# Performance work log

Measured on AMD Instinct MI355X. Metric: run time of the kernel, lower is better.

## Reference

```python
import jax, jax.numpy as jnp
import numpy as np
from jax import lax

B, DIM, H, W = 2, 64, 64, 64
HEADS = 4  # hardcoded in FuseNet (SpectralBlock(dim,4), RestormerBlock(dim,4))
EPS_LN = 1e-5


def pw(x, w, b=None):
    # 1x1 conv, NCHW; w: (out, in)
    y = jnp.einsum('bihw,oi->bohw', x, w)
    return y if b is None else y + b[None, :, None, None]


def dw(x, w, b=None):
    # depthwise 3x3 conv; w: (C, 1, 3, 3)
    y = lax.conv_general_dilated(x, w, (1, 1), 'SAME',
                                 feature_group_count=x.shape[1],
                                 dimension_numbers=('NCHW', 'OIHW', 'NCHW'))
    return y if b is None else y + b[None, :, None, None]


def ln_biasfree(x, w):
    # BiasFree_LayerNorm over channel dim of NCHW (matches to_3d -> var over c)
    mu = jnp.mean(x, axis=1, keepdims=True)
    var = jnp.mean((x - mu) ** 2, axis=1, keepdims=True)
    return x / jnp.sqrt(var + EPS_LN) * w[None, :, None, None]


def ffn(x, in_w, dw_w, out_w):
    # FeedForward: 1x1 -> dw3x3 -> chunk -> gelu gate -> 1x1 (all bias=False)
    h2 = dw(pw(x, in_w), dw_w)
    x1, x2 = jnp.split(h2, 2, axis=1)
    return pw(jax.nn.gelu(x1, approximate=False) * x2, out_w)


def restormer_attn(x, qkv_w, qkv_dw_w, proj_w, temp):
    b, c, h, w = x.shape
    qkv = dw(pw(x, qkv_w), qkv_dw_w)
    q, k, v = jnp.split(qkv, 3, axis=1)
    rs = lambda t: t.reshape(b, HEADS, c // HEADS, h * w)
    q, k, v = rs(q), rs(k), rs(v)
    q = q / jnp.maximum(jnp.linalg.norm(q, axis=-1, keepdims=True), 1e-12)
    k = k / jnp.maximum(jnp.linalg.norm(k, axis=-1, keepdims=True), 1e-12)
    attn = jax.nn.softmax(jnp.einsum('bhcn,bhdn->bhcd', q, k) * temp[None], axis=-1)
    out = jnp.einsum('bhcd,bhdn->bhcn', attn, v).reshape(b, c, h, w)
    return pw(out, proj_w)


def cross_attn(q4, k4, v4, qw, qb, kw, kb, vw, vb, ow, ob):
    b, c, h, w = q4.shape
    n, hd = h * w, c // HEADS
    tok = lambda t: t.reshape(b, c, n).transpose(0, 2, 1)  # b n c
    Q = (jnp.einsum('bnc,oc->bno', tok(q4), qw) + qb).reshape(b, n, HEADS, hd)
    K = (jnp.einsum('bnc,oc->bno', tok(k4), kw) + kb).reshape(b, n, HEADS, hd)
    V = (jnp.einsum('bnc,oc->bno', tok(v4), vw) + vb).reshape(b, n, HEADS, hd)
    energy = jnp.einsum('bqhd,bkhd->bhqk', Q, K)
    attn = jax.nn.softmax(energy / jnp.sqrt(jnp.float32(hd)), axis=-1)
    out = jnp.einsum('bhqk,bkhd->bqhd', attn, V).reshape(b, n, c)
    out = jnp.einsum('bnc,oc->bno', out, ow) + ob
    return out.transpose(0, 2, 1).reshape(b, c, h, w)


def setup_inputs() -> dict:
    key = jax.random.key(0)
    ks = jax.random.split(key, 48)
    d = DIM
    nrm = lambda i, shape, s=0.05: (jax.random.normal(ks[i], shape, jnp.float32) * s)
    inp = {
        'hsi_f0': nrm(0, (B, d, H, W), 1.0),
        'msi_f0': nrm(1, (B, d, H, W), 1.0),
        'hsi_fi': nrm(2, (B, d, H, W), 1.0),
        'msi_fi': nrm(3, (B, d, H, W), 1.0),
        # FuseNet score MLPs (1x1 convs, bias=True)
        'sp_mlp_w': nrm(4, (d, 1)), 'sp_mlp_b': nrm(5, (d,)),
        'spe_mlp_w': nrm(6, (d, d)), 'spe_mlp_b': nrm(7, (d,)),
        # spatial/spectral conv branches (bias=True defaults)
        'spa_dw_w': nrm(8, (d, 1, 3, 3)), 'spa_dw_b': nrm(9, (d,)),
        'spa_pw_w': nrm(10, (d, d)), 'spa_pw_b': nrm(11, (d,)),
        'spe_dw_w': nrm(12, (d, 1, 3, 3)), 'spe_dw_b': nrm(13, (d,)),
        'spe_pw_w': nrm(14, (d, d)), 'spe_pw_b': nrm(15, (d,)),
        # SpectralBlock: CrossAttention linears (bias=True) + norm2 + FFN (bias=False)
        'sb_q_w': nrm(16, (d, d)), 'sb_q_b': nrm(17, (d,)),
        'sb_k_w': nrm(18, (d, d)), 'sb_k_b': nrm(19, (d,)),
        'sb_v_w': nrm(20, (d, d)), 'sb_v_b': nrm(21, (d,)),
        'sb_o_w': nrm(22, (d, d)), 'sb_o_b': nrm(23, (d,)),
        'sb_norm2_w': jnp.ones((d,), jnp.float32),
        'sb_ffn_in_w': nrm(24, (2 * d, d)),
        'sb_ffn_dw_w': nrm(25, (2 * d, 1, 3, 3)),
        'sb_ffn_out_w': nrm(26, (d, d)),
        # RestormerBlock
        'rb_norm1_w': jnp.ones((d,), jnp.float32),
        'rb_temp': jnp.ones((HEADS, 1, 1), jnp.float32),
        'rb_qkv_w': nrm(27, (3 * d, d)),
        'rb_qkv_dw_w': nrm(28, (3 * d, 1, 3, 3)),
        'rb_proj_w': nrm(29, (d, d)),
        'rb_norm2_w': jnp.ones((d,), jnp.float32),
        'rb_ffn_in_w': nrm(30, (2 * d, d)),
        'rb_ffn_dw_w': nrm(31, (2 * d, 1, 3, 3)),
        'rb_ffn_out_w': nrm(32, (d, d)),
    }
    return inp


def reference(hsi_f0, msi_f0, hsi_fi, msi_fi,
              sp_mlp_w, sp_mlp_b, spe_mlp_w, spe_mlp_b,
              spa_dw_w, spa_dw_b, spa_pw_w, spa_pw_b,
              spe_dw_w, spe_dw_b, spe_pw_w, spe_pw_b,
              sb_q_w, sb_q_b, sb_k_w, sb_k_b, sb_v_w, sb_v_b, sb_o_w, sb_o_b,
              sb_norm2_w, sb_ffn_in_w, sb_ffn_dw_w, sb_ffn_out_w,
              rb_norm1_w, rb_temp, rb_qkv_w, rb_qkv_dw_w, rb_proj_w,
              rb_norm2_w, rb_ffn_in_w, rb_ffn_dw_w, rb_ffn_out_w):
    relu6 = lambda t: jnp.clip(t, 0.0, 6.0)
    # spectral score: global max-pool over HW, 1x1 conv, relu6
    spectral_score = jnp.max(hsi_fi, axis=(2, 3), keepdims=True)
    spectral_score = relu6(pw(spectral_score, spe_mlp_w, spe_mlp_b))
    # spatial score: channel mean, 1x1 conv (1->dim), relu6
    spatial_score = jnp.mean(msi_fi, axis=1, keepdims=True)
    spatial_score = relu6(pw(spatial_score, sp_mlp_w, sp_mlp_b))
    # spectral branch on hsi_f0
    hsi = dw(hsi_f0, spe_dw_w, spe_dw_b)
    hsi = hsi + jnp.clip(spectral_score, -1.0, 1.0)
    hsi = pw(hsi, spe_pw_w, spe_pw_b)
    # spatial branch on msi_f0
    msi = dw(msi_f0, spa_dw_w, spa_dw_b)
    msi = msi + jnp.clip(spatial_score, -1.0, 1.0)
    msi = pw(msi, spa_pw_w, spa_pw_b)
    # SpectralBlock: x = cross_attn(q,k,v) + q; x = x + ffn(ln(x))
    x1 = cross_attn(msi, hsi, hsi, sb_q_w, sb_q_b, sb_k_w, sb_k_b,
                    sb_v_w, sb_v_b, sb_o_w, sb_o_b) + msi
    x1 = x1 + ffn(ln_biasfree(x1, sb_norm2_w), sb_ffn_in_w, sb_ffn_dw_w, sb_ffn_out_w)
    # RestormerBlock on msi + hsi
    y = msi + hsi
    y = y + restormer_attn(ln_biasfree(y, rb_norm1_w), rb_qkv_w, rb_qkv_dw_w, rb_proj_w, rb_temp)
    x2 = y + ffn(ln_biasfree(y, rb_norm2_w), rb_ffn_in_w, rb_ffn_dw_w, rb_ffn_out_w)
    return x1 + x2
```

## Files before the change

### kernel.cpp

```cpp
#include <hip/hip_runtime.h>
#include <hip/hip_bf16.h>

#define NB 2
#define NC 64
#define NHW 4096
#define NPIX (NB*NHW)
#define SZ   (NB*NC*NHW)

typedef __attribute__((ext_vector_type(8))) short bf16x8;
typedef __attribute__((ext_vector_type(4))) float f32x4;
typedef __hip_bfloat16 hbf;

__device__ __forceinline__ float clamp01(float v){ return fminf(fmaxf(v, 0.f), 1.f); }

__global__ __launch_bounds__(256) void k_max_hw(const float* __restrict__ in, float* __restrict__ mx){
  int bc = blockIdx.x; int t = threadIdx.x;
  const float* p = in + (size_t)bc*NHW;
  float m = -1e30f;
  for (int n = t; n < NHW; n += 256) m = fmaxf(m, p[n]);
  #pragma unroll
  for (int off = 32; off; off >>= 1) m = fmaxf(m, __shfl_xor(m, off));
  __shared__ float sm[4];
  if ((t & 63) == 0) sm[t >> 6] = m;
  __syncthreads();
  if (t == 0) mx[bc] = fmaxf(fmaxf(sm[0], sm[1]), fmaxf(sm[2], sm[3]));
}

__global__ void k_spe_score(const float* __restrict__ mx, const float* __restrict__ w,
                            const float* __restrict__ bias, float* __restrict__ out){
  int t = threadIdx.x; if (t >= 128) return;
  int b = t >> 6, o = t & 63;
  float acc = bias[o];
  const float* m = mx + b*64;
  for (int i = 0; i < 64; ++i) acc += w[o*64 + i] * m[i];
  out[t] = clamp01(acc);
}

__global__ __launch_bounds__(256) void k_chmean(const float* __restrict__ in, float* __restrict__ out){
  int p = blockIdx.x*256 + threadIdx.x;
  int b = p >> 12, n = p & 4095;
  const float* base = in + (size_t)b*NC*NHW + n;
  float s = 0.f;
  #pragma unroll
  for (int c = 0; c < 64; ++c) s += base[c*NHW];
  out[p] = s * (1.0f/64.0f);
}

__global__ __launch_bounds__(256) void k_dw3b(const float* __restrict__ in0, const float* __restrict__ w0,
    const float* __restrict__ b0, const float* __restrict__ add_bc,
    const float* __restrict__ in1, const float* __restrict__ w1, const float* __restrict__ b1,
    const float* __restrict__ chmean, const float* __restrict__ spw, const float* __restrict__ spb,
    float* __restrict__ out0, float* __restrict__ out1){
  int bb = blockIdx.x;
  int br = bb >= (SZ/256);
  int g = (br ? bb - SZ/256 : bb)*256 + threadIdx.x;
  const float* in = br ? in1 : in0;
  const float* w  = br ? w1  : w0;
  const float* bs = br ? b1  : b0;
  float* out      = br ? out1 : out0;
  int pix = g & 4095; int c = (g >> 12) & 63; int b = g >> 18;
  int y = pix >> 6, x = pix & 63;
  const float* base = in + (size_t)(b*64 + c)*NHW;
  float wf[9];
  #pragma unroll
  for (int i = 0; i < 9; ++i) wf[i] = w[c*9 + i];
  float acc = 0.f;
  #pragma unroll
  for (int ky = -1; ky <= 1; ++ky){
    int yy = y + ky; if ((unsigned)yy >= 64u) continue;
    #pragma unroll
    for (int kx = -1; kx <= 1; ++kx){
      int xx = x + kx; if ((unsigned)xx >= 64u) continue;
      acc += base[yy*64 + xx] * wf[(ky+1)*3 + (kx+1)];
    }
  }
  acc += bs[c];
  if (!br) acc += add_bc[b*64 + c];
  else{
    float z = spw[c] * chmean[b*4096 + pix] + spb[c];
    acc += clamp01(z);
  }
  out[g] = acc;
}

__global__ __launch_bounds__(256) void k_pw(const float* __restrict__ in, const float* __restrict__ w,
    const float* __restrict__ bias, const float* __restrict__ lnw,
    const float* __restrict__ in2, float* __restrict__ add_out,
    const float* __restrict__ r1, const float* __restrict__ r2,
    float* __restrict__ outf, int OC,
    hbf* __restrict__ tq, float tscale, hbf* __restrict__ cq,
    const float* __restrict__ Pacc, const float* __restrict__ Pm, const float* __restrict__ Pl){
  __shared__ __align__(16) float Xs[64][32];
  __shared__ __align__(16) float Wt[64][64];
  __shared__ float psum[8][32], psqs[8][32];
  __shared__ float invs[32];
  __shared__ float fs[4][4][32];
  int t = threadIdx.x;
  int ptile = blockIdx.x; int oc0 = blockIdx.y*64;
  int b = ptile >> 7; int n0 = (ptile & 127)*32;
  const float* inb = in ? in + (size_t)b*64*NHW + n0 : nullptr;
  const float* inb2 = in2 ? in2 + (size_t)b*64*NHW + n0 : nullptr;
  float* aob = add_out ? add_out + (size_t)b*64*NHW + n0 : nullptr;
  if (Pacc){
    if (t < 128){
      int h = t >> 5, n = t & 31;
      int bh = b*4 + h, q = n0 + n;
      float mv[4], lv[4]; float mn = -1e30f;
      #pragma unroll
      for (int c = 0; c < 4; ++c){
        mv[c] = Pm[(size_t)(c*8+bh)*4096 + q];
        lv[c] = Pl[(size_t)(c*8+bh)*4096 + q];
        mn = fmaxf(mn, mv[c]);
      }
      float f[4]; float L = 0.f;
      #pragma unroll
      for (int c = 0; c < 4; ++c){ f[c] = __expf(mv[c]-mn); L += lv[c]*f[c]; }
      float inv = 1.0f / L;
      #pragma unroll
      for (int c = 0; c < 4; ++c) fs[c][h][n] = f[c]*inv;
    }
    __syncthreads();
  }
  float ps = 0.f, pss = 0.f;
  #pragma unroll
  for (int k = 0; k < 8; ++k){
    int i = k*8 + (t >> 5); int n = t & 31;
    float v;
    if (Pacc){
      int h = i >> 4, d = i & 15, bh = b*4 + h;
      const float* pb = Pacc + ((size_t)(bh*16 + d))*4096 + n0 + n;
      v = pb[0]*fs[0][h][n] + pb[(size_t)SZ]*fs[1][h][n]
        + pb[(size_t)2*SZ]*fs[2][h][n] + pb[(size_t)3*SZ]*fs[3][h][n];
    } else {
      v = inb[(size_t)i*NHW + n];
      if (inb2) v += inb2[(size_t)i*NHW + n];
    }
    Xs[i][n] = v;
    if (aob && blockIdx.y == 0) aob[(size_t)i*NHW + n] = v;
    ps += v; pss += v*v;
  }
  if (lnw){ psum[t>>5][t&31] = ps; psqs[t>>5][t&31] = pss; }
  #pragma unroll
  for (int k = 0; k < 16; ++k){
    int idx = k*256 + t; int o = idx & 63, i = idx >> 6;
    float wv = w[(oc0 + o)*64 + i];
    if (lnw) wv *= lnw[i];
    Wt[i][o] = wv;
  }
  __syncthreads();
  if (lnw){
    if (t < 32){
      float s1 = 0.f, s2 = 0.f;
      #pragma unroll
      for (int g = 0; g < 8; ++g){ s1 += psum[g][t]; s2 += psqs[g][t]; }
      float mu = s1*(1.0f/64.0f);
      float var = s2*(1.0f/64.0f) - mu*mu;
      invs[t] = rsqrtf(fmaxf(var, 0.f) + 1e-5f);
    }
    __syncthreads();
  }
  int tn = t & 15, to = t >> 4;
  float a0x=0,a0y=0,a1x=0,a1y=0,a2x=0,a2y=0,a3x=0,a3y=0;
  #pragma unroll
  for (int i = 0; i < 64; ++i){
    const float2 xv = *(const float2*)&Xs[i][tn*2];
    const float4 wv = *(const float4*)&Wt[i][to*4];
    a0x += wv.x*xv.x; a0y += wv.x*xv.y;
    a1x += wv.y*xv.x; a1y += wv.y*xv.y;
    a2x += wv.z*xv.x; a2y += wv.z*xv.y;
    a3x += wv.w*xv.x; a3y += wv.w*xv.y;
  }
  float sx = 1.f, sy = 1.f;
  if (lnw){ sx = invs[tn*2+0]; sy = invs[tn*2+1]; }
  float ax[4] = {a0x,a1x,a2x,a3x}, ay[4] = {a0y,a1y,a2y,a3y};
  #pragma unroll
  for (int oo = 0; oo < 4; ++oo){
    int o = oc0 + to*4 + oo;
    float bv = bias ? bias[o] : 0.f;
    size_t obase = ((size_t)b*OC + o)*NHW + n0 + tn*2;
    float v0 = ax[oo]*sx + bv, v1 = ay[oo]*sy + bv;
    if (r1){ v0 += r1[obase+0]; v1 += r1[obase+1]; }
    if (r2){ v0 += r2[obase+0]; v1 += r2[obase+1]; }
    if (tq){
      int h = o >> 4, d = o & 15;
      size_t tb = ((size_t)(b*4 + h)*4096 + n0 + tn*2)*16 + d;
      tq[tb]    = __float2bfloat16(v0*tscale);
      tq[tb+16] = __float2bfloat16(v1*tscale);
    }
    if (cq){
      cq[obase+0] = __float2bfloat16(v0);
      cq[obase+1] = __float2bfloat16(v1);
    }
    if (outf){
      float2 vv; vv.x = v0; vv.y = v1;
      *(float2*)(outf + obase) = vv;
    }
  }
}

__global__ __launch_bounds__(256) void k_mfa(const hbf* __restrict__ Qt, const hbf* __restrict__ Kt,
                                             const hbf* __restrict__ Vb, float* __restrict__ Pacc,
                                             float* __restrict__ Pm, float* __restrict__ Pl){
  int blk = blockIdx.x;
  int qt = blk & 63; int bh = (blk >> 6) & 7; int c = blk >> 9;
  int t = threadIdx.x;
  int w = t >> 6, l = t & 63;
  int lg = l >> 4, lq = l & 15;
  int q0 = qt*64 + w*16;
  int rho = ((lq >> 2) << 3) + (lq & 3);
  bf16x8 qf = {};
  if (lg < 2) qf = *(const bf16x8*)&Qt[((size_t)bh*4096 + q0 + lq)*16 + lg*8];
  f32x4 acc = {0.f, 0.f, 0.f, 0.f};
  float m = -1e30f, lsum = 0.f;
  const hbf* Ktb = Kt + ((size_t)bh*4096 + c*1024)*16;
  const hbf* Vbb = Vb + (size_t)bh*16*4096 + c*1024;
  for (int kb = 0; kb < 1024; kb += 32){
    bf16x8 kf0 = {}, kf1 = {};
    if (lg < 2){
      kf0 = *(const bf16x8*)&Ktb[(size_t)(kb + rho)*16 + lg*8];
      kf1 = *(const bf16x8*)&Ktb[(size_t)(kb + rho + 4)*16 + lg*8];
    }
    f32x4 z = {0.f, 0.f, 0.f, 0.f};
    f32x4 s0 = __builtin_amdgcn_mfma_f32_16x16x32_bf16(kf0, qf, z, 0, 0, 0);
    f32x4 s1 = __builtin_amdgcn_mfma_f32_16x16x32_bf16(kf1, qf, z, 0, 0, 0);
    float p[8];
    p[0]=s0[0]; p[1]=s0[1]; p[2]=s0[2]; p[3]=s0[3];
    p[4]=s1[0]; p[5]=s1[1]; p[6]=s1[2]; p[7]=s1[3];
    float cm = p[0];
    #pragma unroll
    for (int i = 1; i < 8; ++i) cm = fmaxf(cm, p[i]);
    cm = fmaxf(cm, __shfl_xor(cm, 16));
    cm = fmaxf(cm, __shfl_xor(cm, 32));
    if (!__all(cm <= m + 8.f)){
      float mn = fmaxf(m, cm);
      float f = __expf(m - mn);
      lsum *= f;
      acc[0] *= f; acc[1] *= f; acc[2] *= f; acc[3] *= f;
      m = mn;
    }
    float psum_ = 0.f;
    #pragma unroll
    for (int i = 0; i < 8; ++i){ p[i] = __expf(p[i]-m); psum_ += p[i]; }
    psum_ += __shfl_xor(psum_, 16);
    psum_ += __shfl_xor(psum_, 32);
    lsum += psum_;
    bf16x8 pf;
    #pragma unroll
    for (int j = 0; j < 8; ++j){
      hbf hb = __float2bfloat16(p[j]);
      pf[j] = *reinterpret_cast<short*>(&hb);
    }
    bf16x8 vf = *(const bf16x8*)&Vbb[(size_t)lq*4096 + kb + lg*8];
    acc = __builtin_amdgcn_mfma_f32_16x16x32_bf16(vf, pf, acc, 0, 0, 0);
  }
  int pb = c*8 + bh;
  if (lg == 0){
    Pm[(size_t)pb*4096 + q0 + lq] = m;
    Pl[(size_t)pb*4096 + q0 + lq] = lsum;
  }
  #pragma unroll
  for (int r = 0; r < 4; ++r){
    int d = lg*4 + r;
    Pacc[((size_t)pb*16 + d)*4096 + q0 + lq] = acc[r];
  }
}

__global__ __launch_bounds__(256) void k_dwgate(const float* __restrict__ in, const float* __restrict__ w,
                                                float* __restrict__ out){
  int g = blockIdx.x*256 + threadIdx.x;
  int pix = g & 4095; int c = (g >> 12) & 63; int b = g >> 18;
  int y = pix >> 6, x = pix & 63;
  const float* p1 = in + ((size_t)b*128 + c)*NHW;
  const float* p2 = in + ((size_t)b*128 + 64 + c)*NHW;
  float w1[9], w2[9];
  #pragma unroll
  for (int i = 0; i < 9; ++i){ w1[i] = w[c*9+i]; w2[i] = w[(64+c)*9+i]; }
  float a = 0.f, bb = 0.f;
  #pragma unroll
  for (int ky = -1; ky <= 1; ++ky){
    int yy = y + ky; if ((unsigned)yy >= 64u) continue;
    #pragma unroll
    for (int kx = -1; kx <= 1; ++kx){
      int xx = x + kx; if ((unsigned)xx >= 64u) continue;
      int off = yy*64 + xx; int wi = (ky+1)*3 + (kx+1);
      a  += p1[off]*w1[wi];
      bb += p2[off]*w2[wi];
    }
  }
  float gl = 0.5f*a*(1.0f + erff(a*0.70710678118654752f));
  out[g] = gl*bb;
}

__global__ __launch_bounds__(256) void k_dw192(const float* __restrict__ in, const float* __restrict__ w,
                                               float* __restrict__ out){
  int g = blockIdx.x*256 + threadIdx.x;
  int pix = g & 4095; int bc = g >> 12; int c = bc % 192;
  int y = pix >> 6, x = pix & 63;
  const float* p = in + (size_t)bc*NHW;
  float wf[9];
  #pragma unroll
  for (int i = 0; i < 9; ++i) wf[i] = w[c*9+i];
  float acc = 0.f;
  #pragma unroll
  for (int ky = -1; ky <= 1; ++ky){
    int yy = y + ky; if ((unsigned)yy >= 64u) continue;
    #pragma unroll
    for (int kx = -1; kx <= 1; ++kx){
      int xx = x + kx; if ((unsigned)xx >= 64u) continue;
      acc += p[yy*64 + xx]*wf[(ky+1)*3 + (kx+1)];
    }
  }
  out[g] = acc;
}

__global__ __launch_bounds__(256) void k_rnorm(const float* __restrict__ qkv, float* __restrict__ norms){
  int blk = blockIdx.x; int b = blk >> 7, r = blk & 127;
  int t = threadIdx.x;
  const float* p = qkv + ((size_t)b*192 + r)*NHW;
  float ss = 0.f;
  for (int i = t*4; i < NHW; i += 1024){
    float4 v = *(const float4*)(p + i);
    ss += v.x*v.x + v.y*v.y + v.z*v.z + v.w*v.w;
  }
  #pragma unroll
  for (int off = 32; off; off >>= 1) ss += __shfl_xor(ss, off);
  __shared__ float sm[4];
  if ((t & 63) == 0) sm[t >> 6] = ss;
  __syncthreads();
  if (t == 0) norms[blk] = fmaxf(sqrtf(sm[0]+sm[1]+sm[2]+sm[3]), 1e-12f);
}

__global__ __launch_bounds__(256) void k_rattn2(const float* __restrict__ qkv, const float* __restrict__ norms,
                                                const float* __restrict__ temp, float* __restrict__ out){
  int blk = blockIdx.x; int rq = blk & 15, h = (blk >> 4) & 3, b = blk >> 6;
  int t = threadIdx.x;
  const float* bq = qkv + ((size_t)b*192 + h*16 + rq)*NHW;
  const float* bk = qkv + ((size_t)b*192 + 64 + h*16)*NHW;
  float p[16];
  #pragma unroll
  for (int rk = 0; rk < 16; ++rk) p[rk] = 0.f;
  for (int n = t*4; n < NHW; n += 1024){
    float4 qv4 = *(const float4*)(bq + n);
    #pragma unroll
    for (int rk = 0; rk < 16; ++rk){
      float4 kv = *(const float4*)(bk + (size_t)rk*NHW + n);
      p[rk] += qv4.x*kv.x + qv4.y*kv.y + qv4.z*kv.z + qv4.w*kv.w;
    }
  }
  #pragma unroll
  for (int rk = 0; rk < 16; ++rk)
    #pragma unroll
    for (int off = 32; off; off >>= 1) p[rk] += __shfl_xor(p[rk], off);
  __shared__ float red[4][16];
  if ((t & 63) == 0){
    int wv_ = t >> 6;
    #pragma unroll
    for (int rk = 0; rk < 16; ++rk) red[wv_][rk] = p[rk];
  }
  __syncthreads();
  __shared__ float attn[16];
  if (t == 0){
    float nq = norms[b*128 + h*16 + rq];
    float tp = temp[h];
    float e[16]; float mm = -1e30f;
    #pragma unroll
    for (int rk = 0; rk < 16; ++rk){
      float dot = red[0][rk]+red[1][rk]+red[2][rk]+red[3][rk];
      e[rk] = dot/(nq*norms[b*128 + 64 + h*16 + rk]) * tp;
      mm = fmaxf(mm, e[rk]);
    }
    float ssum = 0.f;
    #pragma unroll
    for (int rk = 0; rk < 16; ++rk){ e[rk] = __expf(e[rk]-mm); ssum += e[rk]; }
    float is = 1.f/ssum;
    #pragma unroll
    for (int rk = 0; rk < 16; ++rk) attn[rk] = e[rk]*is;
  }
  __syncthreads();
  float aw[16];
  #pragma unroll
  for (int rk = 0; rk < 16; ++rk) aw[rk] = attn[rk];
  const float* vb = qkv + ((size_t)b*192 + 128 + h*16)*NHW;
  float* ob = out + ((size_t)b*64 + h*16 + rq)*NHW;
  for (int n = t*4; n < NHW; n += 1024){
    float4 o; o.x = 0.f; o.y = 0.f; o.z = 0.f; o.w = 0.f;
    #pragma unroll
    for (int rk = 0; rk < 16; ++rk){
      float4 v = *(const float4*)(vb + (size_t)rk*NHW + n);
      o.x += aw[rk]*v.x; o.y += aw[rk]*v.y; o.z += aw[rk]*v.z; o.w += aw[rk]*v.w;
    }
    *(float4*)(ob + n) = o;
  }
}

extern "C" void kernel_launch(void* const* d_in, const int* in_sizes, int n_in,
                              void* d_out, int out_size, void* d_ws, size_t ws_size,
                              hipStream_t stream){
  const float* hsi_f0     = (const float*)d_in[0];
  const float* msi_f0     = (const float*)d_in[1];
  const float* hsi_fi     = (const float*)d_in[2];
  const float* msi_fi     = (const float*)d_in[3];
  const float* sp_mlp_w   = (const float*)d_in[4];
  const float* sp_mlp_b   = (const float*)d_in[5];
  const float* spe_mlp_w  = (const float*)d_in[6];
  const float* spe_mlp_b  = (const float*)d_in[7];
  const float* spa_dw_w   = (const float*)d_in[8];
  const float* spa_dw_b   = (const float*)d_in[9];
  const float* spa_pw_w   = (const float*)d_in[10];
  const float* spa_pw_b   = (const float*)d_in[11];
  const float* spe_dw_w   = (const float*)d_in[12];
  const float* spe_dw_b   = (const float*)d_in[13];
  const float* spe_pw_w   = (const float*)d_in[14];
  const float* spe_pw_b   = (const float*)d_in[15];
  const float* sb_q_w     = (const float*)d_in[16];
  const float* sb_q_b     = (const float*)d_in[17];
  const float* sb_k_w     = (const float*)d_in[18];
  const float* sb_k_b     = (const float*)d_in[19];
  const float* sb_v_w     = (const float*)d_in[20];
  const float* sb_v_b     = (const float*)d_in[21];
  const float* sb_o_w     = (const float*)d_in[22];
  const float* sb_o_b     = (const float*)d_in[23];
  const float* sb_norm2_w = (const float*)d_in[24];
  const float* sb_ffn_in_w  = (const float*)d_in[25];
  const float* sb_ffn_dw_w  = (const float*)d_in[26];
  const float* sb_ffn_out_w = (const float*)d_in[27];
  const float* rb_norm1_w = (const float*)d_in[28];
  const float* rb_temp    = (const float*)d_in[29];
  const float* rb_qkv_w   = (const float*)d_in[30];
  const float* rb_qkv_dw_w= (const float*)d_in[31];
  const float* rb_proj_w  = (const float*)d_in[32];
  const float* rb_norm2_w = (const float*)d_in[33];
  const float* rb_ffn_in_w  = (const float*)d_in[34];
  const float* rb_ffn_dw_w  = (const float*)d_in[35];
  const float* rb_ffn_out_w = (const float*)d_in[36];

  float* W   = (float*)d_ws;
  float* Hb  = W;
  float* Mb  = W + (size_t)SZ;
  float* Xb  = W + (size_t)2*SZ;
  float* Yb  = W + (size_t)3*SZ;
  float* T1  = W + (size_t)4*SZ;
  float* QKV = T1;
  float* TB  = W + (size_t)7*SZ;
  float* Tm  = TB;
  float* TB2 = W + (size_t)9*SZ;
  float* Pacc= W + (size_t)7*SZ;
  float* Pm  = W + (size_t)11*SZ;
  float* Pl  = W + (size_t)11*SZ + 131072;
  float* mxb = W + (size_t)12*SZ;
  float* speb= mxb + 128;
  float* cmb = speb + 128;
  float* normb = W + (size_t)12*SZ + 9216;
  hbf* Qt  = (hbf*)(W + (size_t)5*SZ);
  hbf* Kt  = Qt + (size_t)8*4096*16;
  hbf* Vbf = Kt + (size_t)8*4096*16;

  float* outf = (float*)d_out;

  k_max_hw  <<<NB*NC, 256, 0, stream>>>(hsi_fi, mxb);
  k_spe_score<<<1, 128, 0, stream>>>(mxb, spe_mlp_w, spe_mlp_b, speb);
  k_chmean  <<<NPIX/256, 256, 0, stream>>>(msi_fi, cmb);
  k_dw3b<<<2*SZ/256, 256, 0, stream>>>(hsi_f0, spe_dw_w, spe_dw_b, speb,
                                       msi_f0, spa_dw_w, spa_dw_b, cmb, sp_mlp_w, sp_mlp_b,
                                       T1, Tm);
  k_pw<<<dim3(NPIX/32,1), 256, 0, stream>>>(T1, spe_pw_w, spe_pw_b, nullptr, nullptr, nullptr, nullptr, nullptr, Hb, 64, nullptr, 1.f, nullptr, nullptr, nullptr, nullptr);
  k_pw<<<dim3(NPIX/32,1), 256, 0, stream>>>(Tm, spa_pw_w, spa_pw_b, nullptr, nullptr, nullptr, nullptr, nullptr, Mb, 64, nullptr, 1.f, nullptr, nullptr, nullptr, nullptr);
  k_pw<<<dim3(NPIX/32,1), 256, 0, stream>>>(Mb, sb_q_w, sb_q_b, nullptr, nullptr, nullptr, nullptr, nullptr, nullptr, 64, Qt, 0.25f, nullptr, nullptr, nullptr, nullptr);
  k_pw<<<dim3(NPIX/32,1), 256, 0, stream>>>(Hb, sb_k_w, sb_k_b, nullptr, nullptr, nullptr, nullptr, nullptr, nullptr, 64, Kt, 1.f, nullptr, nullptr, nullptr, nullptr);
  k_pw<<<dim3(NPIX/32,1), 256, 0, stream>>>(Hb, sb_v_w, sb_v_b, nullptr, nullptr, nullptr, nullptr, nullptr, nullptr, 64, nullptr, 1.f, Vbf, nullptr, nullptr, nullptr);
  k_mfa<<<2048, 256, 0, stream>>>(Qt, Kt, Vbf, Pacc, Pm, Pl);
  k_pw<<<dim3(NPIX/32,1), 256, 0, stream>>>(nullptr, sb_o_w, sb_o_b, nullptr, nullptr, nullptr, Mb, nullptr, Xb, 64, nullptr, 1.f, nullptr, Pacc, Pm, Pl);
  k_pw<<<dim3(NPIX/32,2), 256, 0, stream>>>(Xb, sb_ffn_in_w, nullptr, sb_norm2_w, nullptr, nullptr, nullptr, nullptr, TB, 128, nullptr, 1.f, nullptr, nullptr, nullptr, nullptr);
  k_dwgate<<<SZ/256, 256, 0, stream>>>(TB, sb_ffn_dw_w, T1);
  k_pw<<<dim3(NPIX/32,1), 256, 0, stream>>>(T1, sb_ffn_out_w, nullptr, nullptr, nullptr, nullptr, Xb, nullptr, Xb, 64, nullptr, 1.f, nullptr, nullptr, nullptr, nullptr);
  k_pw<<<dim3(NPIX/32,3), 256, 0, stream>>>(Hb, rb_qkv_w, nullptr, rb_norm1_w, Mb, Yb, nullptr, nullptr, TB2, 192, nullptr, 1.f, nullptr, nullptr, nullptr, nullptr);
  k_dw192<<<3*SZ/256, 256, 0, stream>>>(TB2, rb_qkv_dw_w, QKV);
  k_rnorm<<<256, 256, 0, stream>>>(QKV, normb);
  k_rattn2<<<128, 256, 0, stream>>>(QKV, normb, rb_temp, TB);
  k_pw<<<dim3(NPIX/32,1), 256, 0, stream>>>(TB, rb_proj_w, nullptr, nullptr, nullptr, nullptr, Yb, nullptr, Yb, 64, nullptr, 1.f, nullptr, nullptr, nullptr, nullptr);
  k_pw<<<dim3(NPIX/32,2), 256, 0, stream>>>(Yb, rb_ffn_in_w, nullptr, rb_norm2_w, nullptr, nullptr, nullptr, nullptr, TB, 128, nullptr, 1.f, nullptr, nullptr, nullptr, nullptr);
  k_dwgate<<<SZ/256, 256, 0, stream>>>(TB, rb_ffn_dw_w, T1);
  k_pw<<<dim3(NPIX/32,1), 256, 0, stream>>>(T1, rb_ffn_out_w, nullptr, nullptr, nullptr, nullptr, Xb, Yb, outf, 64, nullptr, 1.f, nullptr, nullptr, nullptr, nullptr);
}
```

Measured before the change: 276.8 us.

## Batch independent pointwise and depthwise launches, fold spectral MLP, use exp2 softmax

Independent 1x1-conv jobs are grouped into single launches through a job struct indexed by blockIdx.z: the two branch projections, the Q/K/V projections, and the SB FFN-in with the RB QKV projection. The FFN depthwise gate and the 192-channel depthwise conv are merged into one kernel, and the spectral-score MLP is computed inside the depthwise kernel, removing a one-block launch. Softmax now uses exp2f, with log2(e) folded into the Q scale and the rescale threshold. This is meant to cut launch count and fill the GPU better with small grids. The cost is redundant per-thread MLP dot products and buffer reuse (G1 aliases Mb) that must not conflict.

```diff
diff --git a/kernel.cpp b/kernel.cpp
--- a/kernel.cpp
+++ b/kernel.cpp
@@ -6,6 +6,7 @@
 #define NHW 4096
 #define NPIX (NB*NHW)
 #define SZ   (NB*NC*NHW)
+#define LOG2E 1.4426950408889634f
 
 typedef __attribute__((ext_vector_type(8))) short bf16x8;
 typedef __attribute__((ext_vector_type(4))) float f32x4;
@@ -26,16 +27,6 @@
   if (t == 0) mx[bc] = fmaxf(fmaxf(sm[0], sm[1]), fmaxf(sm[2], sm[3]));
 }
 
-__global__ void k_spe_score(const float* __restrict__ mx, const float* __restrict__ w,
-                            const float* __restrict__ bias, float* __restrict__ out){
-  int t = threadIdx.x; if (t >= 128) return;
-  int b = t >> 6, o = t & 63;
-  float acc = bias[o];
-  const float* m = mx + b*64;
-  for (int i = 0; i < 64; ++i) acc += w[o*64 + i] * m[i];
-  out[t] = clamp01(acc);
-}
-
 __global__ __launch_bounds__(256) void k_chmean(const float* __restrict__ in, float* __restrict__ out){
   int p = blockIdx.x*256 + threadIdx.x;
   int b = p >> 12, n = p & 4095;
@@ -46,19 +37,23 @@
   out[p] = s * (1.0f/64.0f);
 }
 
-__global__ __launch_bounds__(256) void k_dw3b(const float* __restrict__ in0, const float* __restrict__ w0,
-    const float* __restrict__ b0, const float* __restrict__ add_bc,
-    const float* __restrict__ in1, const float* __restrict__ w1, const float* __restrict__ b1,
-    const float* __restrict__ chmean, const float* __restrict__ spw, const float* __restrict__ spb,
+__global__ __launch_bounds__(256) void k_dw3b(const float* __restrict__ hsi0, const float* __restrict__ wh,
+    const float* __restrict__ bh, const float* __restrict__ mxb,
+    const float* __restrict__ spe_w, const float* __restrict__ spe_b,
+    const float* __restrict__ msi0, const float* __restrict__ wm, const float* __restrict__ bm,
+    const float* __restrict__ cmb, const float* __restrict__ spw, const float* __restrict__ spb,
     float* __restrict__ out0, float* __restrict__ out1){
   int bb = blockIdx.x;
   int br = bb >= (SZ/256);
-  int g = (br ? bb - SZ/256 : bb)*256 + threadIdx.x;
-  const float* in = br ? in1 : in0;
-  const float* w  = br ? w1  : w0;
-  const float* bs = br ? b1  : b0;
+  int bbl = br ? bb - SZ/256 : bb;
+  int b = bbl >> 10;
+  int c = (bbl >> 4) & 63;
+  int t = threadIdx.x;
+  int pix = (bbl & 15)*256 + t;
+  const float* in = br ? msi0 : hsi0;
+  const float* w  = br ? wm : wh;
+  const float* bs = br ? bm : bh;
   float* out      = br ? out1 : out0;
-  int pix = g & 4095; int c = (g >> 12) & 63; int b = g >> 18;
   int y = pix >> 6, x = pix & 63;
   const float* base = in + (size_t)(b*64 + c)*NHW;
   float wf[9];
@@ -75,32 +70,40 @@
     }
   }
   acc += bs[c];
-  if (!br) acc += add_bc[b*64 + c];
-  else{
-    float z = spw[c] * chmean[b*4096 + pix] + spb[c];
+  if (!br){
+    float spe = spe_b[c];
+    #pragma unroll 8
+    for (int i = 0; i < 64; ++i) spe += spe_w[c*64 + i] * mxb[b*64 + i];
+    acc += clamp01(spe);
+  } else {
+    float z = spw[c] * cmb[b*4096 + pix] + spb[c];
     acc += clamp01(z);
   }
-  out[g] = acc;
-}
-
-__global__ __launch_bounds__(256) void k_pw(const float* __restrict__ in, const float* __restrict__ w,
-    const float* __restrict__ bias, const float* __restrict__ lnw,
-    const float* __restrict__ in2, float* __restrict__ add_out,
-    const float* __restrict__ r1, const float* __restrict__ r2,
-    float* __restrict__ outf, int OC,
-    hbf* __restrict__ tq, float tscale, hbf* __restrict__ cq,
-    const float* __restrict__ Pacc, const float* __restrict__ Pm, const float* __restrict__ Pl){
+  out[(size_t)(b*64 + c)*NHW + pix] = acc;
+}
+
+struct PwJob {
+  const float *in, *w, *bias, *lnw, *in2;
+  float *add_out;
+  const float *r1, *r2;
+  float *outf;
+  int OC;
+  hbf *tq; float tscale; hbf *cq;
+};
+
+__device__ __forceinline__ void pw_body(const PwJob j,
+    const float* __restrict__ Pacc, const float* __restrict__ Pm, const float* __restrict__ Pl,
+    int ptile, int oc0){
   __shared__ __align__(16) float Xs[64][32];
   __shared__ __align__(16) float Wt[64][64];
   __shared__ float psum[8][32], psqs[8][32];
   __shared__ float invs[32];
   __shared__ float fs[4][4][32];
   int t = threadIdx.x;
-  int ptile = blockIdx.x; int oc0 = blockIdx.y*64;
   int b = ptile >> 7; int n0 = (ptile & 127)*32;
-  const float* inb = in ? in + (size_t)b*64*NHW + n0 : nullptr;
-  const float* inb2 = in2 ? in2 + (size_t)b*64*NHW + n0 : nullptr;
-  float* aob = add_out ? add_out + (size_t)b*64*NHW + n0 : nullptr;
+  const float* inb = j.in ? j.in + (size_t)b*64*NHW + n0 : nullptr;
+  const float* inb2 = j.in2 ? j.in2 + (size_t)b*64*NHW + n0 : nullptr;
+  float* aob = j.add_out ? j.add_out + (size_t)b*64*NHW + n0 : nullptr;
   if (Pacc){
     if (t < 128){
       int h = t >> 5, n = t & 31;
@@ -114,7 +117,7 @@
       }
       float f[4]; float L = 0.f;
       #pragma unroll
-      for (int c = 0; c < 4; ++c){ f[c] = __expf(mv[c]-mn); L += lv[c]*f[c]; }
+      for (int c = 0; c < 4; ++c){ f[c] = exp2f(mv[c]-mn); L += lv[c]*f[c]; }
       float inv = 1.0f / L;
       #pragma unroll
       for (int c = 0; c < 4; ++c) fs[c][h][n] = f[c]*inv;
@@ -136,19 +139,19 @@
       if (inb2) v += inb2[(size_t)i*NHW + n];
     }
     Xs[i][n] = v;
-    if (aob && blockIdx.y == 0) aob[(size_t)i*NHW + n] = v;
+    if (aob && oc0 == 0) aob[(size_t)i*NHW + n] = v;
     ps += v; pss += v*v;
   }
-  if (lnw){ psum[t>>5][t&31] = ps; psqs[t>>5][t&31] = pss; }
+  if (j.lnw){ psum[t>>5][t&31] = ps; psqs[t>>5][t&31] = pss; }
   #pragma unroll
   for (int k = 0; k < 16; ++k){
     int idx = k*256 + t; int o = idx & 63, i = idx >> 6;
-    float wv = w[(oc0 + o)*64 + i];
-    if (lnw) wv *= lnw[i];
+    float wv = j.w[(size_t)(oc0 + o)*64 + i];
+    if (j.lnw) wv *= j.lnw[i];
     Wt[i][o] = wv;
   }
   __syncthreads();
-  if (lnw){
+  if (j.lnw){
     if (t < 32){
       float s1 = 0.f, s2 = 0.f;
       #pragma unroll
@@ -171,31 +174,50 @@
     a3x += wv.w*xv.x; a3y += wv.w*xv.y;
   }
   float sx = 1.f, sy = 1.f;
-  if (lnw){ sx = invs[tn*2+0]; sy = invs[tn*2+1]; }
+  if (j.lnw){ sx = invs[tn*2+0]; sy = invs[tn*2+1]; }
   float ax[4] = {a0x,a1x,a2x,a3x}, ay[4] = {a0y,a1y,a2y,a3y};
   #pragma unroll
   for (int oo = 0; oo < 4; ++oo){
     int o = oc0 + to*4 + oo;
-    float bv = bias ? bias[o] : 0.f;
-    size_t obase = ((size_t)b*OC + o)*NHW + n0 + tn*2;
+    float bv = j.bias ? j.bias[o] : 0.f;
+    size_t obase = ((size_t)b*j.OC + o)*NHW + n0 + tn*2;
     float v0 = ax[oo]*sx + bv, v1 = ay[oo]*sy + bv;
-    if (r1){ v0 += r1[obase+0]; v1 += r1[obase+1]; }
-    if (r2){ v0 += r2[obase+0]; v1 += r2[obase+1]; }
-    if (tq){
+    if (j.r1){ v0 += j.r1[obase+0]; v1 += j.r1[obase+1]; }
+    if (j.r2){ v0 += j.r2[obase+0]; v1 += j.r2[obase+1]; }
+    if (j.tq){
       int h = o >> 4, d = o & 15;
       size_t tb = ((size_t)(b*4 + h)*4096 + n0 + tn*2)*16 + d;
-      tq[tb]    = __float2bfloat16(v0*tscale);
-      tq[tb+16] = __float2bfloat16(v1*tscale);
-    }
-    if (cq){
-      cq[obase+0] = __float2bfloat16(v0);
-      cq[obase+1] = __float2bfloat16(v1);
-    }
-    if (outf){
+      j.tq[tb]    = __float2bfloat16(v0*j.tscale);
+      j.tq[tb+16] = __float2bfloat16(v1*j.tscale);
+    }
+    if (j.cq){
+      j.cq[obase+0] = __float2bfloat16(v0);
+      j.cq[obase+1] = __float2bfloat16(v1);
+    }
+    if (j.outf){
       float2 vv; vv.x = v0; vv.y = v1;
-      *(float2*)(outf + obase) = vv;
-    }
-  }
+      *(float2*)(j.outf + obase) = vv;
+    }
+  }
+}
+
+__global__ __launch_bounds__(256) void k_pw1(PwJob a,
+    const float* __restrict__ Pacc, const float* __restrict__ Pm, const float* __restrict__ Pl){
+  pw_body(a, Pacc, Pm, Pl, blockIdx.x, blockIdx.y*64);
+}
+
+__global__ __launch_bounds__(256) void k_pw2z(PwJob a, PwJob b){
+  PwJob j; if (blockIdx.z == 0) j = a; else j = b;
+  int oc0 = blockIdx.y*64;
+  if (oc0 >= j.OC) return;
+  pw_body(j, nullptr, nullptr, nullptr, blockIdx.x, oc0);
+}
+
+__global__ __launch_bounds__(256) void k_pw3z(PwJob a, PwJob b, PwJob c){
+  PwJob j; if (blockIdx.z == 0) j = a; else if (blockIdx.z == 1) j = b; else j = c;
+  int oc0 = blockIdx.y*64;
+  if (oc0 >= j.OC) return;
+  pw_body(j, nullptr, nullptr, nullptr, blockIdx.x, oc0);
 }
 
 __global__ __launch_bounds__(256) void k_mfa(const hbf* __restrict__ Qt, const hbf* __restrict__ Kt,
@@ -231,16 +253,16 @@
     for (int i = 1; i < 8; ++i) cm = fmaxf(cm, p[i]);
     cm = fmaxf(cm, __shfl_xor(cm, 16));
     cm = fmaxf(cm, __shfl_xor(cm, 32));
-    if (!__all(cm <= m + 8.f)){
+    if (!__all(cm <= m + 8.f*LOG2E)){
       float mn = fmaxf(m, cm);
-      float f = __expf(m - mn);
+      float f = exp2f(m - mn);
       lsum *= f;
       acc[0] *= f; acc[1] *= f; acc[2] *= f; acc[3] *= f;
       m = mn;
     }
     float psum_ = 0.f;
     #pragma unroll
-    for (int i = 0; i < 8; ++i){ p[i] = __expf(p[i]-m); psum_ += p[i]; }
+    for (int i = 0; i < 8; ++i){ p[i] = exp2f(p[i]-m); psum_ += p[i]; }
     psum_ += __shfl_xor(psum_, 16);
     psum_ += __shfl_xor(psum_, 32);
     lsum += psum_;
@@ -265,9 +287,8 @@
   }
 }
 
-__global__ __launch_bounds__(256) void k_dwgate(const float* __restrict__ in, const float* __restrict__ w,
-                                                float* __restrict__ out){
-  int g = blockIdx.x*256 + threadIdx.x;
+__device__ __forceinline__ void dwgate_body(const float* __restrict__ in, const float* __restrict__ w,
+                                            float* __restrict__ out, int g){
   int pix = g & 4095; int c = (g >> 12) & 63; int b = g >> 18;
   int y = pix >> 6, x = pix & 63;
   const float* p1 = in + ((size_t)b*128 + c)*NHW;
@@ -291,26 +312,38 @@
   out[g] = gl*bb;
 }
 
-__global__ __launch_bounds__(256) void k_dw192(const float* __restrict__ in, const float* __restrict__ w,
-                                               float* __restrict__ out){
-  int g = blockIdx.x*256 + threadIdx.x;
-  int pix = g & 4095; int bc = g >> 12; int c = bc % 192;
-  int y = pix >> 6, x = pix & 63;
-  const float* p = in + (size_t)bc*NHW;
-  float wf[9];
-  #pragma unroll
-  for (int i = 0; i < 9; ++i) wf[i] = w[c*9+i];
-  float acc = 0.f;
-  #pragma unroll
-  for (int ky = -1; ky <= 1; ++ky){
-    int yy = y + ky; if ((unsigned)yy >= 64u) continue;
-    #pragma unroll
-    for (int kx = -1; kx <= 1; ++kx){
-      int xx = x + kx; if ((unsigned)xx >= 64u) continue;
-      acc += p[yy*64 + xx]*wf[(ky+1)*3 + (kx+1)];
-    }
-  }
-  out[g] = acc;
+__global__ __launch_bounds__(256) void k_dwgate(const float* __restrict__ in, const float* __restrict__ w,
+                                                float* __restrict__ out){
+  dwgate_body(in, w, out, blockIdx.x*256 + threadIdx.x);
+}
+
+__global__ __launch_bounds__(256) void k_dwg2(const float* __restrict__ inG, const float* __restrict__ wG,
+                                              float* __restrict__ outG,
+                                              const float* __restrict__ inD, const float* __restrict__ wD,
+                                              float* __restrict__ outD){
+  int bb = blockIdx.x;
+  if (bb < SZ/256){
+    dwgate_body(inG, wG, outG, bb*256 + threadIdx.x);
+  } else {
+    int g = (bb - SZ/256)*256 + threadIdx.x;
+    int pix = g & 4095; int bc = g >> 12; int c = bc % 192;
+    int y = pix >> 6, x = pix & 63;
+    const float* p = inD + (size_t)bc*NHW;
+    float wf[9];
+    #pragma unroll
+    for (int i = 0; i < 9; ++i) wf[i] = wD[c*9+i];
+    float acc = 0.f;
+    #pragma unroll
+    for (int ky = -1; ky <= 1; ++ky){
+      int yy = y + ky; if ((unsigned)yy >= 64u) continue;
+      #pragma unroll
+      for (int kx = -1; kx <= 1; ++kx){
+        int xx = x + kx; if ((unsigned)xx >= 64u) continue;
+        acc += p[yy*64 + xx]*wf[(ky+1)*3 + (kx+1)];
+      }
+    }
+    outD[g] = acc;
+  }
 }
 
 __global__ __launch_bounds__(256) void k_rnorm(const float* __restrict__ qkv, float* __restrict__ norms){
@@ -391,6 +424,13 @@
     }
     *(float4*)(ob + n) = o;
   }
+}
+
+static inline PwJob mkjob(const float* in, const float* w, const float* bias, const float* lnw,
+                          const float* in2, float* add_out, const float* r1, const float* r2,
+                          float* outf, int OC, hbf* tq, float tscale, hbf* cq){
+  PwJob j; j.in=in; j.w=w; j.bias=bias; j.lnw=lnw; j.in2=in2; j.add_out=add_out;
+  j.r1=r1; j.r2=r2; j.outf=outf; j.OC=OC; j.tq=tq; j.tscale=tscale; j.cq=cq; return j;
 }
 
 extern "C" void kernel_launch(void* const* d_in, const int* in_sizes, int n_in,
@@ -448,37 +488,49 @@
   float* Pm  = W + (size_t)11*SZ;
   float* Pl  = W + (size_t)11*SZ + 131072;
   float* mxb = W + (size_t)12*SZ;
-  float* speb= mxb + 128;
-  float* cmb = speb + 128;
+  float* cmb = mxb + 256;
   float* normb = W + (size_t)12*SZ + 9216;
   hbf* Qt  = (hbf*)(W + (size_t)5*SZ);
   hbf* Kt  = Qt + (size_t)8*4096*16;
   hbf* Vbf = Kt + (size_t)8*4096*16;
+  float* G1 = Mb;
 
   float* outf = (float*)d_out;
-
-  k_max_hw  <<<NB*NC, 256, 0, stream>>>(hsi_fi, mxb);
-  k_spe_score<<<1, 128, 0, stream>>>(mxb, spe_mlp_w, spe_mlp_b, speb);
-  k_chmean  <<<NPIX/256, 256, 0, stream>>>(msi_fi, cmb);
-  k_dw3b<<<2*SZ/256, 256, 0, stream>>>(hsi_f0, spe_dw_w, spe_dw_b, speb,
+  const float QS = 0.25f*LOG2E;
+
+  k_max_hw<<<NB*NC, 256, 0, stream>>>(hsi_fi, mxb);
+  k_chmean<<<NPIX/256, 256, 0, stream>>>(msi_fi, cmb);
+  k_dw3b<<<2*SZ/256, 256, 0, stream>>>(hsi_f0, spe_dw_w, spe_dw_b, mxb, spe_mlp_w, spe_mlp_b,
                                        msi_f0, spa_dw_w, spa_dw_b, cmb, sp_mlp_w, sp_mlp_b,
                                        T1, Tm);
-  k_pw<<<dim3(NPIX/32,1), 256, 0, stream>>>(T1, spe_pw_w, spe_pw_b, nullptr, nullptr, nullptr, nullptr, nullptr, Hb, 64, nullptr, 1.f, nullptr, nullptr, nullptr, nullptr);
-  k_pw<<<dim3(NPIX/32,1), 256, 0, stream>>>(Tm, spa_pw_w, spa_pw_b, nullptr, nullptr, nullptr, nullptr, nullptr, Mb, 64, nullptr, 1.f, nullptr, nullptr, nullptr, nullptr);
-  k_pw<<<dim3(NPIX/32,1), 256, 0, stream>>>(Mb, sb_q_w, sb_q_b, nullptr, nullptr, nullptr, nullptr, nullptr, nullptr, 64, Qt, 0.25f, nullptr, nullptr, nullptr, nullptr);
-  k_pw<<<dim3(NPIX/32,1), 256, 0, stream>>>(Hb, sb_k_w, sb_k_b, nullptr, nullptr, nullptr, nullptr, nullptr, nullptr, 64, Kt, 1.f, nullptr, nullptr, nullptr, nullptr);
-  k_pw<<<dim3(NPIX/32,1), 256, 0, stream>>>(Hb, sb_v_w, sb_v_b, nullptr, nullptr, nullptr, nullptr, nullptr, nullptr, 64, nullptr, 1.f, Vbf, nullptr, nullptr, nullptr);
+  k_pw2z<<<dim3(NPIX/32,1,2), 256, 0, stream>>>(
+      mkjob(T1, spe_pw_w, spe_pw_b, nullptr, nullptr, nullptr, nullptr, nullptr, Hb, 64, nullptr, 1.f, nullptr),
+      mkjob(Tm, spa_pw_w, spa_pw_b, nullptr, nullptr, nullptr, nullptr, nullptr, Mb, 64, nullptr, 1.f, nullptr));
+  k_pw3z<<<dim3(NPIX/32,1,3), 256, 0, stream>>>(
+      mkjob(Mb, sb_q_w, sb_q_b, nullptr, nullptr, nullptr, nullptr, nullptr, nullptr, 64, Qt, QS, nullptr),
+      mkjob(Hb, sb_k_w, sb_k_b, nullptr, nullptr, nullptr, nullptr, nullptr, nullptr, 64, Kt, 1.f, nullptr),
+      mkjob(Hb, sb_v_w, sb_v_b, nullptr, nullptr, nullptr, nullptr, nullptr, nullptr, 64, nullptr, 1.f, Vbf));
   k_mfa<<<2048, 256, 0, stream>>>(Qt, Kt, Vbf, Pacc, Pm, Pl);
-  k_pw<<<dim3(NPIX/32,1), 256, 0, stream>>>(nullptr, sb_o_w, sb_o_b, nullptr, nullptr, nullptr, Mb, nullptr, Xb, 64, nullptr, 1.f, nullptr, Pacc, Pm, Pl);
-  k_pw<<<dim3(NPIX/32,2), 256, 0, stream>>>(Xb, sb_ffn_in_w, nullptr, sb_norm2_w, nullptr, nullptr, nullptr, nullptr, TB, 128, nullptr, 1.f, nullptr, nullptr, nullptr, nullptr);
-  k_dwgate<<<SZ/256, 256, 0, stream>>>(TB, sb_ffn_dw_w, T1);
-  k_pw<<<dim3(NPIX/32,1), 256, 0, stream>>>(T1, sb_ffn_out_w, nullptr, nullptr, nullptr, nullptr, Xb, nullptr, Xb, 64, nullptr, 1.f, nullptr, nullptr, nullptr, nullptr);
-  k_pw<<<dim3(NPIX/32,3), 256, 0, stream>>>(Hb, rb_qkv_w, nullptr, rb_norm1_w, Mb, Yb, nullptr, nullptr, TB2, 192, nullptr, 1.f, nullptr, nullptr, nullptr, nullptr);
-  k_dw192<<<3*SZ/256, 256, 0, stream>>>(TB2, rb_qkv_dw_w, QKV);
+  k_pw1<<<dim3(NPIX/32,1), 256, 0, stream>>>(
+      mkjob(nullptr, sb_o_w, sb_o_b, nullptr, nullptr, nullptr, Mb, nullptr, Xb, 64, nullptr, 1.f, nullptr),
+      Pacc, Pm, Pl);
+  k_pw2z<<<dim3(NPIX/32,3,2), 256, 0, stream>>>(
+      mkjob(Xb, sb_ffn_in_w, nullptr, sb_norm2_w, nullptr, nullptr, nullptr, nullptr, TB, 128, nullptr, 1.f, nullptr),
+      mkjob(Hb, rb_qkv_w, nullptr, rb_norm1_w, Mb, Yb, nullptr, nullptr, TB2, 192, nullptr, 1.f, nullptr));
+  k_dwg2<<<SZ/256 + 3*SZ/256, 256, 0, stream>>>(TB, sb_ffn_dw_w, G1, TB2, rb_qkv_dw_w, QKV);
+  k_pw1<<<dim3(NPIX/32,1), 256, 0, stream>>>(
+      mkjob(G1, sb_ffn_out_w, nullptr, nullptr, nullptr, nullptr, Xb, nullptr, Xb, 64, nullptr, 1.f, nullptr),
+      nullptr, nullptr, nullptr);
   k_rnorm<<<256, 256, 0, stream>>>(QKV, normb);
   k_rattn2<<<128, 256, 0, stream>>>(QKV, normb, rb_temp, TB);
-  k_pw<<<dim3(NPIX/32,1), 256, 0, stream>>>(TB, rb_proj_w, nullptr, nullptr, nullptr, nullptr, Yb, nullptr, Yb, 64, nullptr, 1.f, nullptr, nullptr, nullptr, nullptr);
-  k_pw<<<dim3(NPIX/32,2), 256, 0, stream>>>(Yb, rb_ffn_in_w, nullptr, rb_norm2_w, nullptr, nullptr, nullptr, nullptr, TB, 128, nullptr, 1.f, nullptr, nullptr, nullptr, nullptr);
+  k_pw1<<<dim3(NPIX/32,1), 256, 0, stream>>>(
+      mkjob(TB, rb_proj_w, nullptr, nullptr, nullptr, nullptr, Yb, nullptr, Yb, 64, nullptr, 1.f, nullptr),
+      nullptr, nullptr, nullptr);
+  k_pw1<<<dim3(NPIX/32,2), 256, 0, stream>>>(
+      mkjob(Yb, rb_ffn_in_w, nullptr, rb_norm2_w, nullptr, nullptr, nullptr, nullptr, TB, 128, nullptr, 1.f, nullptr),
+      nullptr, nullptr, nullptr);
   k_dwgate<<<SZ/256, 256, 0, stream>>>(TB, rb_ffn_dw_w, T1);
-  k_pw<<<dim3(NPIX/32,1), 256, 0, stream>>>(T1, rb_ffn_out_w, nullptr, nullptr, nullptr, nullptr, Xb, Yb, outf, 64, nullptr, 1.f, nullptr, nullptr, nullptr, nullptr);
-}
+  k_pw1<<<dim3(NPIX/32,1), 256, 0, stream>>>(
+      mkjob(T1, rb_ffn_out_w, nullptr, nullptr, nullptr, nullptr, Xb, Yb, outf, 64, nullptr, 1.f, nullptr),
+      nullptr, nullptr, nullptr);
+}
```

New measurement: 263.8 us. -4.7%, faster.
